# Kernel tuning notes

Hardware: AMD Instinct MI355X
Metric: run time of the kernel (lower is better)

## Reference

```python
import jax, jax.numpy as jnp
import numpy as np

ALPHA = 0.9     # projection strength
EPS = 1e-3      # Lyapunov positive-definite regularizer (lyapunov_eps)
B, D, H = 32768, 512, 64


def setup_inputs() -> dict:
    key = jax.random.key(0)
    ks = jax.random.split(key, 8)
    def w(k, shape, fan_in):
        return jax.random.normal(k, shape, jnp.float32) * (1.0 / fan_in) ** 0.5
    return dict(
        x=jax.random.normal(ks[0], (B, D), jnp.float32),
        # dynamics MLP f(x): D -> 64 -> 64 -> D
        W1=w(ks[1], (D, H), D), b1=jnp.zeros((H,), jnp.float32),
        W2=w(ks[2], (H, H), H), b2=jnp.zeros((H,), jnp.float32),
        W3=w(ks[3], (H, D), H), b3=jnp.zeros((D,), jnp.float32),
        # Lyapunov MLP V(z): D -> 64 -> 64 -> 1 (+ eps*||z||^2)
        V1=w(ks[4], (D, H), D), c1=jnp.zeros((H,), jnp.float32),
        V2=w(ks[5], (H, H), H), c2=jnp.zeros((H,), jnp.float32),
        V3=w(ks[6], (H, 1), H), c3=jnp.zeros((1,), jnp.float32),
    )


def reference(x, W1, b1, W2, b2, W3, b3, V1, c1, V2, c2, V3, c3):
    def fnet(xx):  # nominal dynamics: [B,D] -> [B,D]
        h = jax.nn.relu(xx @ W1 + b1)
        h = jax.nn.relu(h @ W2 + b2)
        return h @ W3 + b3

    def vnet(z):  # Lyapunov candidate: [B,D] -> [B]
        h = jax.nn.relu(z @ V1 + c1)
        h = jax.nn.relu(h @ V2 + c2)
        return (h @ V3 + c3)[..., 0] + EPS * jnp.sum(z * z, axis=-1)

    def lyap_sum(xx):
        v = vnet(fnet(xx))
        return jnp.sum(v), v

    # grad_v replicates the in-forward lyapunov.backward(...): dV(f(x))/dx, shape [B,D]
    (_, lyap), grad_v = jax.value_and_grad(lyap_sum, has_aux=True)(x)

    f = fnet(x)                                   # [B, D]
    dot = jnp.sum(grad_v * grad_v, axis=-1)       # bmm(gv, fv): per-sample <grad_v, grad_v>
    denom = jnp.sum(grad_v * grad_v)              # global .pow(2).sum() over all elements
    orth = jax.nn.relu(dot + ALPHA * lyap) / denom  # [B]
    return f - orth[:, None] * grad_v             # diag_embed(orth) @ grad_v
```

## Files before the change

### kernel.cpp

```cpp
#include <hip/hip_runtime.h>

#define ALPHA_C 0.9f
#define EPS_C 1e-3f

typedef unsigned short u16;
typedef __attribute__((ext_vector_type(8))) short short8;
typedef __attribute__((ext_vector_type(4))) short short4v;
typedef __attribute__((ext_vector_type(4))) float f32x4;
#define MFMA(a, b, c) __builtin_amdgcn_mfma_f32_16x16x32_bf16(a, b, c, 0, 0, 0)
#define LDS_FENCE() asm volatile("" ::: "memory")

__device__ __forceinline__ u16 f2bf(float f) {
  union { float f; unsigned u; } v; v.f = f;
  unsigned u = v.u;
  u += 0x7FFFu + ((u >> 16) & 1u);
  return (u16)(u >> 16);
}
__device__ __forceinline__ float bf2f(u16 h) {
  union { unsigned u; float f; } v; v.u = ((unsigned)h) << 16;
  return v.f;
}

__global__ __launch_bounds__(256) void k_conv(
    const float* __restrict__ W1, const float* __restrict__ W2, const float* __restrict__ W3,
    const float* __restrict__ V1, const float* __restrict__ V2,
    u16* __restrict__ PW1T, u16* __restrict__ PW1n, u16* __restrict__ PV1T, u16* __restrict__ PV1n,
    u16* __restrict__ PW3T, u16* __restrict__ PW3n, u16* __restrict__ PW2T, u16* __restrict__ PW2n,
    u16* __restrict__ PV2T, u16* __restrict__ PV2n) {
  int i = blockIdx.x * 256 + threadIdx.x;
  {
    int k = i >> 6, j = i & 63;
    u16 b = f2bf(W1[i]);
    PW1T[((((j >> 4) * 16 + (k >> 5)) * 4 + ((k & 31) >> 3)) * 16 + (j & 15)) * 8 + (k & 7)] = b;
    PW1n[((((k >> 4) * 2 + (j >> 5)) * 4 + ((j & 31) >> 3)) * 16 + (k & 15)) * 8 + (j & 7)] = b;
    u16 c = f2bf(V1[i]);
    PV1T[((((j >> 4) * 16 + (k >> 5)) * 4 + ((k & 31) >> 3)) * 16 + (j & 15)) * 8 + (k & 7)] = c;
    PV1n[((((k >> 4) * 2 + (j >> 5)) * 4 + ((j & 31) >> 3)) * 16 + (k & 15)) * 8 + (j & 7)] = c;
  }
  {
    int k = i >> 9, n = i & 511;
    u16 b = f2bf(W3[i]);
    PW3T[((((n >> 4) * 2 + (k >> 5)) * 4 + ((k & 31) >> 3)) * 16 + (n & 15)) * 8 + (k & 7)] = b;
    PW3n[((((k >> 4) * 16 + (n >> 5)) * 4 + ((n & 31) >> 3)) * 16 + (k & 15)) * 8 + (n & 7)] = b;
  }
  if (i < 4096) {
    int k = i >> 6, j = i & 63;
    u16 b = f2bf(W2[i]);
    PW2T[((((j >> 4) * 2 + (k >> 5)) * 4 + ((k & 31) >> 3)) * 16 + (j & 15)) * 8 + (k & 7)] = b;
    PW2n[((((k >> 4) * 2 + (j >> 5)) * 4 + ((j & 31) >> 3)) * 16 + (k & 15)) * 8 + (j & 7)] = b;
    u16 c = f2bf(V2[i]);
    PV2T[((((j >> 4) * 2 + (k >> 5)) * 4 + ((k & 31) >> 3)) * 16 + (j & 15)) * 8 + (k & 7)] = c;
    PV2n[((((k >> 4) * 2 + (j >> 5)) * 4 + ((j & 31) >> 3)) * 16 + (k & 15)) * 8 + (j & 7)] = c;
  }
}

__global__ __launch_bounds__(256, 2) void k_fused(
    const float* __restrict__ x,
    const u16* __restrict__ PW1T, const float* __restrict__ b1,
    const u16* __restrict__ PW2T, const float* __restrict__ b2,
    const u16* __restrict__ PW3T, const float* __restrict__ b3,
    const u16* __restrict__ PV1T, const float* __restrict__ c1,
    const u16* __restrict__ PV2T, const u16* __restrict__ PV2n, const float* __restrict__ c2,
    const float* __restrict__ V3, const float* __restrict__ c3,
    const u16* __restrict__ PV1n, const u16* __restrict__ PW3n,
    const u16* __restrict__ PW2n, const u16* __restrict__ PW1n,
    u16* __restrict__ FP, u16* __restrict__ T2P,
    float* __restrict__ NUM, float* __restrict__ DP) {
  __shared__ u16 H1s[64 * 72];
  __shared__ u16 H2s[64 * 72];
  __shared__ u16 S2s[64 * 72];
  __shared__ u16 As[64 * 136];
  __shared__ float dred[4];
  const int tid = threadIdx.x;
  const int lane = tid & 63, w = tid >> 6, q = lane >> 4, r = lane & 15;
  const int m0 = blockIdx.x * 64;
  const int arow = w * 16 + r;
  const int strip = blockIdx.x * 4 + w;
  const int h = lane >> 5, c4 = lane & 31;
  const float* xbase = x + (size_t)(m0 + w * 16) * 512;

  f32x4 acc1[4] = {};
  float4 xr0[8], xr1[8];

#define LOAD_X(regs, kc)                                                        \
  _Pragma("unroll") for (int it = 0; it < 8; ++it)                              \
    regs[it] = *(const float4*)&xbase[(it * 2 + h) * 512 + (kc) * 128 + c4 * 4];

#define STAGE_X(regs)                                                           \
  _Pragma("unroll") for (int it = 0; it < 8; ++it) {                            \
    float4 v = regs[it];                                                        \
    short4v s4;                                                                 \
    s4[0] = (short)f2bf(v.x); s4[1] = (short)f2bf(v.y);                         \
    s4[2] = (short)f2bf(v.z); s4[3] = (short)f2bf(v.w);                         \
    *(short4v*)&As[(w * 16 + it * 2 + h) * 136 + c4 * 4] = s4;                  \
  }

#define MFMA_X(kc)                                                              \
  _Pragma("unroll") for (int ks = 0; ks < 4; ++ks) {                            \
    short8 a = *(const short8*)&As[arow * 136 + ks * 32 + q * 8];               \
    _Pragma("unroll") for (int t = 0; t < 4; ++t) {                             \
      short8 b = *(const short8*)&PW1T[((t * 16 + (kc) * 4 + ks) * 64 + lane) * 8]; \
      acc1[t] = MFMA(a, b, acc1[t]);                                            \
    }                                                                           \
  }

  LOAD_X(xr0, 0)
  STAGE_X(xr0) LDS_FENCE(); LOAD_X(xr1, 1) MFMA_X(0) LDS_FENCE();
  STAGE_X(xr1) LDS_FENCE(); LOAD_X(xr0, 2) MFMA_X(1) LDS_FENCE();
  STAGE_X(xr0) LDS_FENCE(); LOAD_X(xr1, 3) MFMA_X(2) LDS_FENCE();
  STAGE_X(xr1) LDS_FENCE(); MFMA_X(3)

  #pragma unroll
  for (int t = 0; t < 4; ++t) {
    int col = t * 16 + r; float bv = b1[col];
    #pragma unroll
    for (int g = 0; g < 4; ++g) {
      float hh = acc1[t][g] + bv; hh = hh > 0.f ? hh : 0.f;
      H1s[(w * 16 + q * 4 + g) * 72 + col] = f2bf(hh);
    }
  }
  LDS_FENCE();

  f32x4 acc2[4] = {};
  #pragma unroll
  for (int ks = 0; ks < 2; ++ks) {
    short8 a = *(const short8*)&H1s[arow * 72 + ks * 32 + q * 8];
    #pragma unroll
    for (int t = 0; t < 4; ++t) {
      short8 b = *(const short8*)&PW2T[((t * 2 + ks) * 64 + lane) * 8];
      acc2[t] = MFMA(a, b, acc2[t]);
    }
  }
  #pragma unroll
  for (int t = 0; t < 4; ++t) {
    int col = t * 16 + r; float bv = b2[col];
    #pragma unroll
    for (int g = 0; g < 4; ++g) {
      float hh = acc2[t][g] + bv; hh = hh > 0.f ? hh : 0.f;
      H2s[(w * 16 + q * 4 + g) * 72 + col] = f2bf(hh);
    }
  }
  LDS_FENCE();

  f32x4 g1acc[4] = {};
  float ssq[4] = {0.f, 0.f, 0.f, 0.f};
  #pragma unroll 1
  for (int nc = 0; nc < 4; ++nc) {
    f32x4 facc[8] = {};
    #pragma unroll
    for (int ks = 0; ks < 2; ++ks) {
      short8 a = *(const short8*)&H2s[arow * 72 + ks * 32 + q * 8];
      #pragma unroll
      for (int t = 0; t < 8; ++t) {
        short8 b = *(const short8*)&PW3T[(((nc * 8 + t) * 2 + ks) * 64 + lane) * 8];
        facc[t] = MFMA(a, b, facc[t]);
      }
    }
    #pragma unroll
    for (int t = 0; t < 8; ++t) {
      float bv = b3[nc * 128 + t * 16 + r];
      short4v s4;
      #pragma unroll
      for (int g = 0; g < 4; ++g) {
        float v = facc[t][g] + bv;
        ssq[g] += v * v;
        u16 bb = f2bf(v);
        As[(w * 16 + q * 4 + g) * 136 + t * 16 + r] = bb;
        s4[g] = (short)bb;
      }
      *(short4v*)&FP[(size_t)(((strip * 4 + nc) * 8 + t) * 64 + lane) * 4] = s4;
    }
    LDS_FENCE();
    #pragma unroll
    for (int ks = 0; ks < 4; ++ks) {
      short8 a = *(const short8*)&As[arow * 136 + ks * 32 + q * 8];
      #pragma unroll
      for (int t = 0; t < 4; ++t) {
        short8 b = *(const short8*)&PV1T[((t * 16 + nc * 4 + ks) * 64 + lane) * 8];
        g1acc[t] = MFMA(a, b, g1acc[t]);
      }
    }
    LDS_FENCE();
  }

  f32x4 g1v[4];
  #pragma unroll
  for (int t = 0; t < 4; ++t) {
    int col = t * 16 + r; float cv = c1[col];
    #pragma unroll
    for (int g = 0; g < 4; ++g) {
      float v = g1acc[t][g] + cv; v = v > 0.f ? v : 0.f;
      g1v[t][g] = v;
      S2s[(w * 16 + q * 4 + g) * 72 + col] = f2bf(v);
    }
  }
  LDS_FENCE();
  f32x4 g2acc[4] = {};
  #pragma unroll
  for (int ks = 0; ks < 2; ++ks) {
    short8 a = *(const short8*)&S2s[arow * 72 + ks * 32 + q * 8];
    #pragma unroll
    for (int t = 0; t < 4; ++t) {
      short8 b = *(const short8*)&PV2T[((t * 2 + ks) * 64 + lane) * 8];
      g2acc[t] = MFMA(a, b, g2acc[t]);
    }
  }
  float tot[4] = {0.f, 0.f, 0.f, 0.f};
  #pragma unroll
  for (int t = 0; t < 4; ++t) {
    int col = t * 16 + r;
    float c2v = c2[col], v3v = V3[col];
    #pragma unroll
    for (int g = 0; g < 4; ++g) {
      float pre = g2acc[t][g] + c2v;
      float g2 = pre > 0.f ? pre : 0.f;
      S2s[(w * 16 + q * 4 + g) * 72 + col] = pre > 0.f ? f2bf(v3v) : (u16)0;
      tot[g] += g2 * v3v;
    }
  }
  LDS_FENCE();
  f32x4 s2acc[4] = {};
  #pragma unroll
  for (int ks = 0; ks < 2; ++ks) {
    short8 a = *(const short8*)&S2s[arow * 72 + ks * 32 + q * 8];
    #pragma unroll
    for (int t = 0; t < 4; ++t) {
      short8 b = *(const short8*)&PV2n[((t * 2 + ks) * 64 + lane) * 8];
      s2acc[t] = MFMA(a, b, s2acc[t]);
    }
  }
  #pragma unroll
  for (int t = 0; t < 4; ++t) {
    int col = t * 16 + r;
    #pragma unroll
    for (int g = 0; g < 4; ++g) {
      float sv = g1v[t][g] > 0.f ? s2acc[t][g] : 0.f;
      S2s[(w * 16 + q * 4 + g) * 72 + col] = f2bf(sv);
    }
  }
  LDS_FENCE();
  float c3v = c3[0];
  float lyap_row[4];
  #pragma unroll
  for (int g = 0; g < 4; ++g) {
    float s = tot[g] + EPS_C * ssq[g];
    s += __shfl_xor(s, 1); s += __shfl_xor(s, 2); s += __shfl_xor(s, 4); s += __shfl_xor(s, 8);
    lyap_row[g] = s + c3v;
  }

  asm volatile("s_waitcnt vmcnt(0)" ::: "memory");

  f32x4 t3acc[4] = {};
  #pragma unroll 1
  for (int nc = 0; nc < 4; ++nc) {
    f32x4 uacc[8] = {};
    #pragma unroll
    for (int ks = 0; ks < 2; ++ks) {
      short8 a = *(const short8*)&S2s[arow * 72 + ks * 32 + q * 8];
      #pragma unroll
      for (int t = 0; t < 8; ++t) {
        short8 b = *(const short8*)&PV1n[(((nc * 8 + t) * 2 + ks) * 64 + lane) * 8];
        uacc[t] = MFMA(a, b, uacc[t]);
      }
    }
    #pragma unroll
    for (int t = 0; t < 8; ++t) {
      short4v f4 = *(const short4v*)&FP[(size_t)(((strip * 4 + nc) * 8 + t) * 64 + lane) * 4];
      #pragma unroll
      for (int g = 0; g < 4; ++g) {
        As[(w * 16 + q * 4 + g) * 136 + t * 16 + r] =
            f2bf(uacc[t][g] + 2.f * EPS_C * bf2f((u16)f4[g]));
      }
    }
    LDS_FENCE();
    #pragma unroll
    for (int ks = 0; ks < 4; ++ks) {
      short8 a = *(const short8*)&As[arow * 136 + ks * 32 + q * 8];
      #pragma unroll
      for (int t = 0; t < 4; ++t) {
        short8 b = *(const short8*)&PW3n[((t * 16 + nc * 4 + ks) * 64 + lane) * 8];
        t3acc[t] = MFMA(a, b, t3acc[t]);
      }
    }
    LDS_FENCE();
  }
  #pragma unroll
  for (int t = 0; t < 4; ++t) {
    int col = t * 16 + r;
    #pragma unroll
    for (int g = 0; g < 4; ++g) {
      int addr = (w * 16 + q * 4 + g) * 72 + col;
      u16 h2 = H2s[addr];
      H2s[addr] = h2 ? f2bf(t3acc[t][g]) : (u16)0;
    }
  }
  LDS_FENCE();
  f32x4 t2acc[4] = {};
  #pragma unroll
  for (int ks = 0; ks < 2; ++ks) {
    short8 a = *(const short8*)&H2s[arow * 72 + ks * 32 + q * 8];
    #pragma unroll
    for (int t = 0; t < 4; ++t) {
      short8 b = *(const short8*)&PW2n[((t * 2 + ks) * 64 + lane) * 8];
      t2acc[t] = MFMA(a, b, t2acc[t]);
    }
  }
  #pragma unroll
  for (int t = 0; t < 4; ++t) {
    int col = t * 16 + r;
    #pragma unroll
    for (int g = 0; g < 4; ++g) {
      int addr = (w * 16 + q * 4 + g) * 72 + col;
      u16 h1 = H1s[addr];
      H1s[addr] = h1 ? f2bf(t2acc[t][g]) : (u16)0;
    }
  }
  LDS_FENCE();
  short8 v0 = *(const short8*)&H1s[arow * 72 + 0 + q * 8];
  short8 v1 = *(const short8*)&H1s[arow * 72 + 32 + q * 8];
  *(short8*)&T2P[(size_t)((strip * 2 + 0) * 64 + lane) * 8] = v0;
  *(short8*)&T2P[(size_t)((strip * 2 + 1) * 64 + lane) * 8] = v1;
  float ssq2[4] = {0.f, 0.f, 0.f, 0.f};
  #pragma unroll 1
  for (int nc = 0; nc < 4; ++nc) {
    f32x4 acc[8] = {};
    #pragma unroll
    for (int t = 0; t < 8; ++t) {
      short8 b0 = *(const short8*)&PW1n[(((nc * 8 + t) * 2 + 0) * 64 + lane) * 8];
      short8 b1 = *(const short8*)&PW1n[(((nc * 8 + t) * 2 + 1) * 64 + lane) * 8];
      acc[t] = MFMA(v0, b0, acc[t]);
      acc[t] = MFMA(v1, b1, acc[t]);
    }
    #pragma unroll
    for (int t = 0; t < 8; ++t)
      #pragma unroll
      for (int g = 0; g < 4; ++g) ssq2[g] += acc[t][g] * acc[t][g];
  }
  float totw = 0.f;
  #pragma unroll
  for (int g = 0; g < 4; ++g) {
    float s = ssq2[g];
    s += __shfl_xor(s, 1); s += __shfl_xor(s, 2); s += __shfl_xor(s, 4); s += __shfl_xor(s, 8);
    if (r == 0) {
      int rowg = m0 + w * 16 + q * 4 + g;
      float nm = s + ALPHA_C * lyap_row[g];
      NUM[rowg] = nm > 0.f ? nm : 0.f;
    }
    s += __shfl_xor(s, 16); s += __shfl_xor(s, 32);
    totw += s;
  }
  if (lane == 0) dred[w] = totw;
  __syncthreads();
  if (tid == 0) atomicAdd(&DP[blockIdx.x & 255], dred[0] + dred[1] + dred[2] + dred[3]);
}

__global__ __launch_bounds__(256) void k_out(
    const u16* __restrict__ T2P, const u16* __restrict__ PW1n,
    const u16* __restrict__ FP, const float* __restrict__ NUM, const float* __restrict__ DP,
    float* __restrict__ out) {
  __shared__ float red[256];
  const int tid = threadIdx.x;
  const int lane = tid & 63, w = tid >> 6, q = lane >> 4, r = lane & 15;
  const int m0 = blockIdx.x * 64;
  const int strip = blockIdx.x * 4 + w;
  red[tid] = DP[tid];
  __syncthreads();
  for (int s = 128; s >= 1; s >>= 1) {
    if (tid < s) red[tid] += red[tid + s];
    __syncthreads();
  }
  const float inv_denom = 1.f / red[0];
  float sc[4];
  #pragma unroll
  for (int g = 0; g < 4; ++g) sc[g] = NUM[m0 + w * 16 + q * 4 + g] * inv_denom;
  short8 a0 = *(const short8*)&T2P[(size_t)((strip * 2 + 0) * 64 + lane) * 8];
  short8 a1 = *(const short8*)&T2P[(size_t)((strip * 2 + 1) * 64 + lane) * 8];
  #pragma unroll 1
  for (int nc = 0; nc < 4; ++nc) {
    f32x4 acc[8] = {};
    #pragma unroll
    for (int t = 0; t < 8; ++t) {
      short8 b0 = *(const short8*)&PW1n[(((nc * 8 + t) * 2 + 0) * 64 + lane) * 8];
      short8 b1 = *(const short8*)&PW1n[(((nc * 8 + t) * 2 + 1) * 64 + lane) * 8];
      acc[t] = MFMA(a0, b0, acc[t]);
      acc[t] = MFMA(a1, b1, acc[t]);
    }
    #pragma unroll
    for (int t = 0; t < 8; ++t) {
      short4v f4 = *(const short4v*)&FP[(size_t)(((strip * 4 + nc) * 8 + t) * 64 + lane) * 4];
      #pragma unroll
      for (int g = 0; g < 4; ++g) {
        out[(size_t)(m0 + w * 16 + q * 4 + g) * 512 + nc * 128 + t * 16 + r] =
            bf2f((u16)f4[g]) - sc[g] * acc[t][g];
      }
    }
  }
}

extern "C" void kernel_launch(void* const* d_in, const int* in_sizes, int n_in,
                              void* d_out, int out_size, void* d_ws, size_t ws_size,
                              hipStream_t stream) {
  const float* x  = (const float*)d_in[0];
  const float* W1 = (const float*)d_in[1];
  const float* b1 = (const float*)d_in[2];
  const float* W2 = (const float*)d_in[3];
  const float* b2 = (const float*)d_in[4];
  const float* W3 = (const float*)d_in[5];
  const float* b3 = (const float*)d_in[6];
  const float* V1 = (const float*)d_in[7];
  const float* c1 = (const float*)d_in[8];
  const float* V2 = (const float*)d_in[9];
  const float* c2 = (const float*)d_in[10];
  const float* V3 = (const float*)d_in[11];
  const float* c3 = (const float*)d_in[12];
  float* out = (float*)d_out;

  u16* FP = (u16*)d_ws;
  float* NUM = (float*)(FP + 16777216);
  float* DP  = NUM + 32768;
  u16* T2P  = (u16*)(DP + 256);
  u16* PW1T = T2P + 2097152;
  u16* PW1n = PW1T + 32768;
  u16* PV1T = PW1n + 32768;
  u16* PV1n = PV1T + 32768;
  u16* PW3T = PV1n + 32768;
  u16* PW3n = PW3T + 32768;
  u16* PW2T = PW3n + 32768;
  u16* PW2n = PW2T + 4096;
  u16* PV2T = PW2n + 4096;
  u16* PV2n = PV2T + 4096;

  hipMemsetAsync(DP, 0, 256 * sizeof(float), stream);

  k_conv<<<128, 256, 0, stream>>>(W1, W2, W3, V1, V2,
                                  PW1T, PW1n, PV1T, PV1n, PW3T, PW3n,
                                  PW2T, PW2n, PV2T, PV2n);
  k_fused<<<512, 256, 0, stream>>>(x, PW1T, b1, PW2T, b2, PW3T, b3, PV1T, c1,
                                   PV2T, PV2n, c2, V3, c3, PV1n, PW3n, PW2n, PW1n,
                                   FP, T2P, NUM, DP);
  k_out<<<512, 256, 0, stream>>>(T2P, PW1n, FP, NUM, DP, out);
}
```

Before: 178.3 us.

## Stage weight fragments in LDS, coalesce output stores, fold DP memset into conv

The fused kernel now cooperatively copies each chunk of packed weight fragments (W1, W3, V1, PV1n, PW3n, PW1n) into a 32KB shared buffer behind block barriers, instead of having every wave re-read them from global memory. A-fragments are hoisted out of the loops. The output kernel prefetches B fragments in double-buffered registers and routes results through an LDS tile so global stores are row-contiguous float4 writes. The DP zeroing memset is folded into the conversion kernel. The cost is extra barriers and more LDS per block, which may reduce occupancy.

```diff
diff --git a/kernel.cpp b/kernel.cpp
--- a/kernel.cpp
+++ b/kernel.cpp
@@ -9,6 +9,9 @@
 typedef __attribute__((ext_vector_type(4))) float f32x4;
 #define MFMA(a, b, c) __builtin_amdgcn_mfma_f32_16x16x32_bf16(a, b, c, 0, 0, 0)
 #define LDS_FENCE() asm volatile("" ::: "memory")
+#define BAR_TOP()    { LDS_FENCE(); __builtin_amdgcn_s_barrier(); LDS_FENCE(); }
+#define BAR_STAGED() { LDS_FENCE(); asm volatile("s_waitcnt lgkmcnt(0)" ::: "memory"); \
+                       __builtin_amdgcn_s_barrier(); LDS_FENCE(); }
 
 __device__ __forceinline__ u16 f2bf(float f) {
   union { float f; unsigned u; } v; v.f = f;
@@ -26,8 +29,9 @@
     const float* __restrict__ V1, const float* __restrict__ V2,
     u16* __restrict__ PW1T, u16* __restrict__ PW1n, u16* __restrict__ PV1T, u16* __restrict__ PV1n,
     u16* __restrict__ PW3T, u16* __restrict__ PW3n, u16* __restrict__ PW2T, u16* __restrict__ PW2n,
-    u16* __restrict__ PV2T, u16* __restrict__ PV2n) {
+    u16* __restrict__ PV2T, u16* __restrict__ PV2n, float* __restrict__ DP) {
   int i = blockIdx.x * 256 + threadIdx.x;
+  if (i < 256) DP[i] = 0.f;
   {
     int k = i >> 6, j = i & 63;
     u16 b = f2bf(W1[i]);
@@ -53,6 +57,20 @@
     PV2n[((((k >> 4) * 2 + (j >> 5)) * 4 + ((j & 31) >> 3)) * 16 + (k & 15)) * 8 + (j & 7)] = c;
   }
 }
+
+#define LDG8(dst, P, FRAG)                                                      \
+  _Pragma("unroll") for (int j = 0; j < 8; ++j)                                 \
+    dst[j] = *(const short8*)&P[((size_t)(FRAG) * 64 + lane) * 8];
+
+#define STAGE16(DST, P, SRCFRAG)                                                \
+  _Pragma("unroll") for (int c = 0; c < 4; ++c)                                 \
+    *(short8*)&Ws[((DST) * 512) + (c * 256 + tid) * 8] =                        \
+      *(const short8*)&P[((size_t)(SRCFRAG) * 512) + (c * 256 + tid) * 8];
+
+#define STAGE4x4(DST, P, OFF)                                                   \
+  _Pragma("unroll") for (int t = 0; t < 4; ++t)                                 \
+    *(short8*)&Ws[((DST) + t * 4) * 512 + tid * 8] =                            \
+      *(const short8*)&P[((size_t)(t * 16 + (OFF))) * 512 + tid * 8];
 
 __global__ __launch_bounds__(256, 2) void k_fused(
     const float* __restrict__ x,
@@ -66,10 +84,11 @@
     const u16* __restrict__ PW2n, const u16* __restrict__ PW1n,
     u16* __restrict__ FP, u16* __restrict__ T2P,
     float* __restrict__ NUM, float* __restrict__ DP) {
-  __shared__ u16 H1s[64 * 72];
-  __shared__ u16 H2s[64 * 72];
-  __shared__ u16 S2s[64 * 72];
-  __shared__ u16 As[64 * 136];
+  __shared__ __align__(16) u16 H1s[64 * 72];
+  __shared__ __align__(16) u16 H2s[64 * 72];
+  __shared__ __align__(16) u16 S2s[64 * 72];
+  __shared__ __align__(16) u16 As[64 * 136];
+  __shared__ __align__(16) u16 Ws[16384];
   __shared__ float dred[4];
   const int tid = threadIdx.x;
   const int lane = tid & 63, w = tid >> 6, q = lane >> 4, r = lane & 15;
@@ -80,36 +99,37 @@
   const float* xbase = x + (size_t)(m0 + w * 16) * 512;
 
   f32x4 acc1[4] = {};
-  float4 xr0[8], xr1[8];
-
-#define LOAD_X(regs, kc)                                                        \
-  _Pragma("unroll") for (int it = 0; it < 8; ++it)                              \
-    regs[it] = *(const float4*)&xbase[(it * 2 + h) * 512 + (kc) * 128 + c4 * 4];
-
-#define STAGE_X(regs)                                                           \
-  _Pragma("unroll") for (int it = 0; it < 8; ++it) {                            \
-    float4 v = regs[it];                                                        \
-    short4v s4;                                                                 \
-    s4[0] = (short)f2bf(v.x); s4[1] = (short)f2bf(v.y);                         \
-    s4[2] = (short)f2bf(v.z); s4[3] = (short)f2bf(v.w);                         \
-    *(short4v*)&As[(w * 16 + it * 2 + h) * 136 + c4 * 4] = s4;                  \
-  }
-
-#define MFMA_X(kc)                                                              \
-  _Pragma("unroll") for (int ks = 0; ks < 4; ++ks) {                            \
-    short8 a = *(const short8*)&As[arow * 136 + ks * 32 + q * 8];               \
-    _Pragma("unroll") for (int t = 0; t < 4; ++t) {                             \
-      short8 b = *(const short8*)&PW1T[((t * 16 + (kc) * 4 + ks) * 64 + lane) * 8]; \
-      acc1[t] = MFMA(a, b, acc1[t]);                                            \
-    }                                                                           \
-  }
-
-  LOAD_X(xr0, 0)
-  STAGE_X(xr0) LDS_FENCE(); LOAD_X(xr1, 1) MFMA_X(0) LDS_FENCE();
-  STAGE_X(xr1) LDS_FENCE(); LOAD_X(xr0, 2) MFMA_X(1) LDS_FENCE();
-  STAGE_X(xr0) LDS_FENCE(); LOAD_X(xr1, 3) MFMA_X(2) LDS_FENCE();
-  STAGE_X(xr1) LDS_FENCE(); MFMA_X(3)
-
+  float4 xr[8];
+  #pragma unroll
+  for (int it = 0; it < 8; ++it)
+    xr[it] = *(const float4*)&xbase[(it * 2 + h) * 512 + c4 * 4];
+  #pragma unroll 1
+  for (int kc = 0; kc < 4; ++kc) {
+    BAR_TOP();
+    STAGE4x4(0, PW1T, kc * 4);
+    #pragma unroll
+    for (int it = 0; it < 8; ++it) {
+      float4 v = xr[it]; short4v s4;
+      s4[0] = (short)f2bf(v.x); s4[1] = (short)f2bf(v.y);
+      s4[2] = (short)f2bf(v.z); s4[3] = (short)f2bf(v.w);
+      *(short4v*)&As[(w * 16 + it * 2 + h) * 136 + c4 * 4] = s4;
+    }
+    if (kc < 3) {
+      #pragma unroll
+      for (int it = 0; it < 8; ++it)
+        xr[it] = *(const float4*)&xbase[(it * 2 + h) * 512 + (kc + 1) * 128 + c4 * 4];
+    }
+    BAR_STAGED();
+    #pragma unroll
+    for (int ks = 0; ks < 4; ++ks) {
+      short8 a = *(const short8*)&As[arow * 136 + ks * 32 + q * 8];
+      #pragma unroll
+      for (int t = 0; t < 4; ++t) {
+        short8 b = *(const short8*)&Ws[((t * 4 + ks) * 64 + lane) * 8];
+        acc1[t] = MFMA(a, b, acc1[t]);
+      }
+    }
+  }
   #pragma unroll
   for (int t = 0; t < 4; ++t) {
     int col = t * 16 + r; float bv = b1[col];
@@ -121,40 +141,46 @@
   }
   LDS_FENCE();
 
-  f32x4 acc2[4] = {};
-  #pragma unroll
-  for (int ks = 0; ks < 2; ++ks) {
-    short8 a = *(const short8*)&H1s[arow * 72 + ks * 32 + q * 8];
-    #pragma unroll
-    for (int t = 0; t < 4; ++t) {
-      short8 b = *(const short8*)&PW2T[((t * 2 + ks) * 64 + lane) * 8];
-      acc2[t] = MFMA(a, b, acc2[t]);
-    }
-  }
-  #pragma unroll
-  for (int t = 0; t < 4; ++t) {
-    int col = t * 16 + r; float bv = b2[col];
-    #pragma unroll
-    for (int g = 0; g < 4; ++g) {
-      float hh = acc2[t][g] + bv; hh = hh > 0.f ? hh : 0.f;
-      H2s[(w * 16 + q * 4 + g) * 72 + col] = f2bf(hh);
+  {
+    short8 a0 = *(const short8*)&H1s[arow * 72 + 0 + q * 8];
+    short8 a1 = *(const short8*)&H1s[arow * 72 + 32 + q * 8];
+    f32x4 acc2[4] = {};
+    #pragma unroll
+    for (int t = 0; t < 4; ++t) {
+      short8 b0 = *(const short8*)&PW2T[((t * 2 + 0) * 64 + lane) * 8];
+      short8 b1 = *(const short8*)&PW2T[((t * 2 + 1) * 64 + lane) * 8];
+      acc2[t] = MFMA(a0, b0, acc2[t]);
+      acc2[t] = MFMA(a1, b1, acc2[t]);
+    }
+    #pragma unroll
+    for (int t = 0; t < 4; ++t) {
+      int col = t * 16 + r; float bv = b2[col];
+      #pragma unroll
+      for (int g = 0; g < 4; ++g) {
+        float hh = acc2[t][g] + bv; hh = hh > 0.f ? hh : 0.f;
+        H2s[(w * 16 + q * 4 + g) * 72 + col] = f2bf(hh);
+      }
     }
   }
   LDS_FENCE();
 
   f32x4 g1acc[4] = {};
   float ssq[4] = {0.f, 0.f, 0.f, 0.f};
+  short8 h2a0 = *(const short8*)&H2s[arow * 72 + 0 + q * 8];
+  short8 h2a1 = *(const short8*)&H2s[arow * 72 + 32 + q * 8];
   #pragma unroll 1
   for (int nc = 0; nc < 4; ++nc) {
+    BAR_TOP();
+    STAGE16(0, PW3T, nc * 16);
+    STAGE4x4(16, PV1T, nc * 4);
+    BAR_STAGED();
     f32x4 facc[8] = {};
     #pragma unroll
-    for (int ks = 0; ks < 2; ++ks) {
-      short8 a = *(const short8*)&H2s[arow * 72 + ks * 32 + q * 8];
-      #pragma unroll
-      for (int t = 0; t < 8; ++t) {
-        short8 b = *(const short8*)&PW3T[(((nc * 8 + t) * 2 + ks) * 64 + lane) * 8];
-        facc[t] = MFMA(a, b, facc[t]);
-      }
+    for (int t = 0; t < 8; ++t) {
+      short8 b0 = *(const short8*)&Ws[((t * 2 + 0) * 64 + lane) * 8];
+      short8 b1 = *(const short8*)&Ws[((t * 2 + 1) * 64 + lane) * 8];
+      facc[t] = MFMA(h2a0, b0, facc[t]);
+      facc[t] = MFMA(h2a1, b1, facc[t]);
     }
     #pragma unroll
     for (int t = 0; t < 8; ++t) {
@@ -176,11 +202,10 @@
       short8 a = *(const short8*)&As[arow * 136 + ks * 32 + q * 8];
       #pragma unroll
       for (int t = 0; t < 4; ++t) {
-        short8 b = *(const short8*)&PV1T[((t * 16 + nc * 4 + ks) * 64 + lane) * 8];
+        short8 b = *(const short8*)&Ws[((16 + t * 4 + ks) * 64 + lane) * 8];
         g1acc[t] = MFMA(a, b, g1acc[t]);
       }
     }
-    LDS_FENCE();
   }
 
   f32x4 g1v[4];
@@ -196,13 +221,15 @@
   }
   LDS_FENCE();
   f32x4 g2acc[4] = {};
-  #pragma unroll
-  for (int ks = 0; ks < 2; ++ks) {
-    short8 a = *(const short8*)&S2s[arow * 72 + ks * 32 + q * 8];
-    #pragma unroll
-    for (int t = 0; t < 4; ++t) {
-      short8 b = *(const short8*)&PV2T[((t * 2 + ks) * 64 + lane) * 8];
-      g2acc[t] = MFMA(a, b, g2acc[t]);
+  {
+    short8 a0 = *(const short8*)&S2s[arow * 72 + 0 + q * 8];
+    short8 a1 = *(const short8*)&S2s[arow * 72 + 32 + q * 8];
+    #pragma unroll
+    for (int t = 0; t < 4; ++t) {
+      short8 b0 = *(const short8*)&PV2T[((t * 2 + 0) * 64 + lane) * 8];
+      short8 b1 = *(const short8*)&PV2T[((t * 2 + 1) * 64 + lane) * 8];
+      g2acc[t] = MFMA(a0, b0, g2acc[t]);
+      g2acc[t] = MFMA(a1, b1, g2acc[t]);
     }
   }
   float tot[4] = {0.f, 0.f, 0.f, 0.f};
@@ -220,13 +247,15 @@
   }
   LDS_FENCE();
   f32x4 s2acc[4] = {};
-  #pragma unroll
-  for (int ks = 0; ks < 2; ++ks) {
-    short8 a = *(const short8*)&S2s[arow * 72 + ks * 32 + q * 8];
-    #pragma unroll
-    for (int t = 0; t < 4; ++t) {
-      short8 b = *(const short8*)&PV2n[((t * 2 + ks) * 64 + lane) * 8];
-      s2acc[t] = MFMA(a, b, s2acc[t]);
+  {
+    short8 a0 = *(const short8*)&S2s[arow * 72 + 0 + q * 8];
+    short8 a1 = *(const short8*)&S2s[arow * 72 + 32 + q * 8];
+    #pragma unroll
+    for (int t = 0; t < 4; ++t) {
+      short8 b0 = *(const short8*)&PV2n[((t * 2 + 0) * 64 + lane) * 8];
+      short8 b1 = *(const short8*)&PV2n[((t * 2 + 1) * 64 + lane) * 8];
+      s2acc[t] = MFMA(a0, b0, s2acc[t]);
+      s2acc[t] = MFMA(a1, b1, s2acc[t]);
     }
   }
   #pragma unroll
@@ -251,25 +280,32 @@
   asm volatile("s_waitcnt vmcnt(0)" ::: "memory");
 
   f32x4 t3acc[4] = {};
+  short8 s2a0 = *(const short8*)&S2s[arow * 72 + 0 + q * 8];
+  short8 s2a1 = *(const short8*)&S2s[arow * 72 + 32 + q * 8];
   #pragma unroll 1
   for (int nc = 0; nc < 4; ++nc) {
+    BAR_TOP();
+    STAGE16(0, PV1n, nc * 16);
+    STAGE4x4(16, PW3n, nc * 4);
+    BAR_STAGED();
+    short4v fpr[8];
+    #pragma unroll
+    for (int t = 0; t < 8; ++t)
+      fpr[t] = *(const short4v*)&FP[(size_t)(((strip * 4 + nc) * 8 + t) * 64 + lane) * 4];
     f32x4 uacc[8] = {};
     #pragma unroll
-    for (int ks = 0; ks < 2; ++ks) {
-      short8 a = *(const short8*)&S2s[arow * 72 + ks * 32 + q * 8];
-      #pragma unroll
-      for (int t = 0; t < 8; ++t) {
-        short8 b = *(const short8*)&PV1n[(((nc * 8 + t) * 2 + ks) * 64 + lane) * 8];
-        uacc[t] = MFMA(a, b, uacc[t]);
-      }
-    }
-    #pragma unroll
-    for (int t = 0; t < 8; ++t) {
-      short4v f4 = *(const short4v*)&FP[(size_t)(((strip * 4 + nc) * 8 + t) * 64 + lane) * 4];
+    for (int t = 0; t < 8; ++t) {
+      short8 b0 = *(const short8*)&Ws[((t * 2 + 0) * 64 + lane) * 8];
+      short8 b1 = *(const short8*)&Ws[((t * 2 + 1) * 64 + lane) * 8];
+      uacc[t] = MFMA(s2a0, b0, uacc[t]);
+      uacc[t] = MFMA(s2a1, b1, uacc[t]);
+    }
+    #pragma unroll
+    for (int t = 0; t < 8; ++t) {
       #pragma unroll
       for (int g = 0; g < 4; ++g) {
         As[(w * 16 + q * 4 + g) * 136 + t * 16 + r] =
-            f2bf(uacc[t][g] + 2.f * EPS_C * bf2f((u16)f4[g]));
+            f2bf(uacc[t][g] + 2.f * EPS_C * bf2f((u16)fpr[t][g]));
       }
     }
     LDS_FENCE();
@@ -278,11 +314,10 @@
       short8 a = *(const short8*)&As[arow * 136 + ks * 32 + q * 8];
       #pragma unroll
       for (int t = 0; t < 4; ++t) {
-        short8 b = *(const short8*)&PW3n[((t * 16 + nc * 4 + ks) * 64 + lane) * 8];
+        short8 b = *(const short8*)&Ws[((16 + t * 4 + ks) * 64 + lane) * 8];
         t3acc[t] = MFMA(a, b, t3acc[t]);
       }
     }
-    LDS_FENCE();
   }
   #pragma unroll
   for (int t = 0; t < 4; ++t) {
@@ -296,13 +331,15 @@
   }
   LDS_FENCE();
   f32x4 t2acc[4] = {};
-  #pragma unroll
-  for (int ks = 0; ks < 2; ++ks) {
-    short8 a = *(const short8*)&H2s[arow * 72 + ks * 32 + q * 8];
-    #pragma unroll
-    for (int t = 0; t < 4; ++t) {
-      short8 b = *(const short8*)&PW2n[((t * 2 + ks) * 64 + lane) * 8];
-      t2acc[t] = MFMA(a, b, t2acc[t]);
+  {
+    short8 a0 = *(const short8*)&H2s[arow * 72 + 0 + q * 8];
+    short8 a1 = *(const short8*)&H2s[arow * 72 + 32 + q * 8];
+    #pragma unroll
+    for (int t = 0; t < 4; ++t) {
+      short8 b0 = *(const short8*)&PW2n[((t * 2 + 0) * 64 + lane) * 8];
+      short8 b1 = *(const short8*)&PW2n[((t * 2 + 1) * 64 + lane) * 8];
+      t2acc[t] = MFMA(a0, b0, t2acc[t]);
+      t2acc[t] = MFMA(a1, b1, t2acc[t]);
     }
   }
   #pragma unroll
@@ -323,11 +360,14 @@
   float ssq2[4] = {0.f, 0.f, 0.f, 0.f};
   #pragma unroll 1
   for (int nc = 0; nc < 4; ++nc) {
+    BAR_TOP();
+    STAGE16(0, PW1n, nc * 16);
+    BAR_STAGED();
     f32x4 acc[8] = {};
     #pragma unroll
     for (int t = 0; t < 8; ++t) {
-      short8 b0 = *(const short8*)&PW1n[(((nc * 8 + t) * 2 + 0) * 64 + lane) * 8];
-      short8 b1 = *(const short8*)&PW1n[(((nc * 8 + t) * 2 + 1) * 64 + lane) * 8];
+      short8 b0 = *(const short8*)&Ws[((t * 2 + 0) * 64 + lane) * 8];
+      short8 b1 = *(const short8*)&Ws[((t * 2 + 1) * 64 + lane) * 8];
       acc[t] = MFMA(v0, b0, acc[t]);
       acc[t] = MFMA(v1, b1, acc[t]);
     }
@@ -354,11 +394,12 @@
   if (tid == 0) atomicAdd(&DP[blockIdx.x & 255], dred[0] + dred[1] + dred[2] + dred[3]);
 }
 
-__global__ __launch_bounds__(256) void k_out(
+__global__ __launch_bounds__(256, 2) void k_out(
     const u16* __restrict__ T2P, const u16* __restrict__ PW1n,
     const u16* __restrict__ FP, const float* __restrict__ NUM, const float* __restrict__ DP,
     float* __restrict__ out) {
   __shared__ float red[256];
+  __shared__ __align__(16) float OutS[64 * 132];
   const int tid = threadIdx.x;
   const int lane = tid & 63, w = tid >> 6, q = lane >> 4, r = lane & 15;
   const int m0 = blockIdx.x * 64;
@@ -375,25 +416,42 @@
   for (int g = 0; g < 4; ++g) sc[g] = NUM[m0 + w * 16 + q * 4 + g] * inv_denom;
   short8 a0 = *(const short8*)&T2P[(size_t)((strip * 2 + 0) * 64 + lane) * 8];
   short8 a1 = *(const short8*)&T2P[(size_t)((strip * 2 + 1) * 64 + lane) * 8];
+  short8 bA[8], bB[8];
+  LDG8(bA, PW1n, ((j >> 1) * 2 + (j & 1)));
   #pragma unroll 1
   for (int nc = 0; nc < 4; ++nc) {
+    LDG8(bB, PW1n, ((nc * 8 + 4 + (j >> 1)) * 2 + (j & 1)));
+    short4v fpr[8];
+    #pragma unroll
+    for (int t = 0; t < 8; ++t)
+      fpr[t] = *(const short4v*)&FP[(size_t)(((strip * 4 + nc) * 8 + t) * 64 + lane) * 4];
     f32x4 acc[8] = {};
     #pragma unroll
-    for (int t = 0; t < 8; ++t) {
-      short8 b0 = *(const short8*)&PW1n[(((nc * 8 + t) * 2 + 0) * 64 + lane) * 8];
-      short8 b1 = *(const short8*)&PW1n[(((nc * 8 + t) * 2 + 1) * 64 + lane) * 8];
-      acc[t] = MFMA(a0, b0, acc[t]);
-      acc[t] = MFMA(a1, b1, acc[t]);
-    }
-    #pragma unroll
-    for (int t = 0; t < 8; ++t) {
-      short4v f4 = *(const short4v*)&FP[(size_t)(((strip * 4 + nc) * 8 + t) * 64 + lane) * 4];
-      #pragma unroll
-      for (int g = 0; g < 4; ++g) {
-        out[(size_t)(m0 + w * 16 + q * 4 + g) * 512 + nc * 128 + t * 16 + r] =
-            bf2f((u16)f4[g]) - sc[g] * acc[t][g];
-      }
-    }
+    for (int t = 0; t < 4; ++t) {
+      acc[t] = MFMA(a0, bA[t * 2 + 0], acc[t]);
+      acc[t] = MFMA(a1, bA[t * 2 + 1], acc[t]);
+    }
+    int ncn = (nc + 1) & 3;
+    LDG8(bA, PW1n, ((ncn * 8 + (j >> 1)) * 2 + (j & 1)));
+    #pragma unroll
+    for (int t = 0; t < 4; ++t) {
+      acc[4 + t] = MFMA(a0, bB[t * 2 + 0], acc[4 + t]);
+      acc[4 + t] = MFMA(a1, bB[t * 2 + 1], acc[4 + t]);
+    }
+    #pragma unroll
+    for (int t = 0; t < 8; ++t) {
+      #pragma unroll
+      for (int g = 0; g < 4; ++g)
+        OutS[(w * 16 + q * 4 + g) * 132 + t * 16 + r] =
+            bf2f((u16)fpr[t][g]) - sc[g] * acc[t][g];
+    }
+    LDS_FENCE();
+    #pragma unroll
+    for (int jj = 0; jj < 8; ++jj) {
+      f32x4 ov = *(const f32x4*)&OutS[(w * 16 + (lane >> 5) + jj * 2) * 132 + (lane & 31) * 4];
+      *(f32x4*)&out[(size_t)(m0 + w * 16 + (lane >> 5) + jj * 2) * 512 + nc * 128 + (lane & 31) * 4] = ov;
+    }
+    LDS_FENCE();
   }
 }
 
@@ -430,11 +488,9 @@
   u16* PV2T = PW2n + 4096;
   u16* PV2n = PV2T + 4096;
 
-  hipMemsetAsync(DP, 0, 256 * sizeof(float), stream);
-
   k_conv<<<128, 256, 0, stream>>>(W1, W2, W3, V1, V2,
                                   PW1T, PW1n, PV1T, PV1n, PW3T, PW3n,
-                                  PW2T, PW2n, PV2T, PV2n);
+                                  PW2T, PW2n, PV2T, PV2n, DP);
   k_fused<<<512, 256, 0, stream>>>(x, PW1T, b1, PW2T, b2, PW3T, b3, PV1T, c1,
                                    PV2T, PV2n, c2, V3, c3, PV1n, PW3n, PW2n, PW1n,
                                    FP, T2P, NUM, DP);
```

Result: faster. 172.8 us (-3.1%).
